# Performance work log

Hardware: AMD Instinct MI355X
Metric: run time of the kernel (lower is better)

The kernel has to match this reference:

```python
import jax, jax.numpy as jnp
import numpy as np

TEMP = 0.07
BATCH, DIM, NUM_ATTRS = 8192, 512, 4
NUM_PROTOS = 2 ** NUM_ATTRS  # all binary combos present => unique() size is static


def setup_inputs() -> dict:
    key = jax.random.key(0)
    z_flowed = jax.random.normal(key, (BATCH, DIM), dtype=jnp.float32)
    # binary attribute combos, all 16 present; first column = MSB (matches torch.unique row sort)
    combo = jnp.arange(BATCH, dtype=jnp.int32) % NUM_PROTOS
    shifts = jnp.arange(NUM_ATTRS - 1, -1, -1, dtype=jnp.int32)
    attributes = ((combo[:, None] >> shifts[None, :]) & 1).astype(jnp.float32)
    return {"z_flowed": z_flowed, "attributes": attributes}


def _l2norm(x, axis=-1, eps=1e-12):
    n = jnp.sqrt(jnp.sum(x * x, axis=axis, keepdims=True))
    return x / jnp.maximum(n, eps)  # F.normalize semantics


def reference(z_flowed, attributes):
    B, D = z_flowed.shape
    num_attrs = attributes.shape[1]
    P = 2 ** num_attrs
    z_norm = _l2norm(z_flowed, axis=1)

    # inverse indices of torch.unique(attributes, dim=0): binary row -> code (MSB = col 0)
    shifts = jnp.arange(num_attrs - 1, -1, -1)
    inverse = jnp.sum((attributes > 0.5).astype(jnp.int32) * (1 << shifts)[None, :], axis=1)

    # prototype = normalized segment-mean of z_norm per attribute combo (detached)
    sums = jax.ops.segment_sum(z_norm, inverse, num_segments=P)          # [P, D]
    counts = jax.ops.segment_sum(jnp.ones((B,), z_norm.dtype), inverse, num_segments=P)
    means = sums / jnp.maximum(counts, 1.0)[:, None]
    prototypes = jax.lax.stop_gradient(_l2norm(means, axis=1))
    prototypes = jnp.where(counts[:, None] > 0, prototypes, 0.0)

    # prototype contrastive term
    proto_sim = (z_norm @ prototypes.T) / TEMP                            # [B, P]
    exp_sim = jnp.exp(proto_sim)
    pos = exp_sim[jnp.arange(B), inverse]
    alls = jnp.maximum(jnp.sum(exp_sim, axis=1), 1e-8)
    loss = -jnp.mean(jnp.log(pos / alls + 1e-8))

    # pairwise term (positives only when BOTH attribute rows are all-ones)
    pairwise = (z_norm @ z_norm.T) / TEMP                                 # [B, B]
    attr_sim = attributes @ attributes.T
    pos_mask = (attr_sim == num_attrs).astype(z_norm.dtype)
    pos_mask = pos_mask * (1.0 - jnp.eye(B, dtype=z_norm.dtype))
    exp_pw = jnp.exp(pairwise)
    pos_sims = jnp.sum(exp_pw * pos_mask, axis=1)
    all_sims = jnp.sum(exp_pw, axis=1) - jnp.diagonal(exp_pw)
    valid = jnp.sum(pos_mask, axis=1) > 0
    per_row = -jnp.log(pos_sims / (all_sims + 1e-8) + 1e-8)
    n_valid = jnp.sum(valid.astype(z_norm.dtype))
    pairwise_loss = jnp.sum(jnp.where(valid, per_row, 0.0)) / jnp.maximum(n_valid, 1.0)
    loss = jnp.where(n_valid > 0, 0.7 * loss + 0.3 * pairwise_loss, loss)
    return loss
```

## Files before the change

### kernel.cpp

```cpp
#include <hip/hip_runtime.h>
#include <math.h>

#define NB 8192
#define ND 512
#define NPROTO 16
#define NBLK 256
#define TINV 14.285714285714286f
#define PW_BLOCKS 256
#define PL_BLOCKS 256

typedef short short8 __attribute__((ext_vector_type(8)));
typedef float float4v __attribute__((ext_vector_type(4)));

__device__ __forceinline__ unsigned short f2bf(float f) {
  unsigned u = __builtin_bit_cast(unsigned, f);
  unsigned r = (u + 0x7FFFu + ((u >> 16) & 1u)) >> 16;
  return (unsigned short)r;
}
__device__ __forceinline__ float bflo(unsigned u) {
  return __builtin_bit_cast(float, u << 16);
}
__device__ __forceinline__ float bfhi(unsigned u) {
  return __builtin_bit_cast(float, u & 0xFFFF0000u);
}

__global__ __launch_bounds__(512) void k_norm(
    const float* __restrict__ z, const float* __restrict__ attr,
    unsigned short* __restrict__ znb, float* __restrict__ partialSum,
    int* __restrict__ code, float* __restrict__ protoSumG)
{
  __shared__ float acc[NPROTO * ND];
  const int t = threadIdx.x, lane = t & 63, wid = t >> 6;
  for (int i = t; i < NPROTO * ND; i += 512) acc[i] = 0.f;
  if (blockIdx.x == 0)
    for (int i = t; i < NPROTO * ND; i += 512) protoSumG[i] = 0.f;
  __syncthreads();
  #pragma unroll
  for (int rr = 0; rr < 4; ++rr) {
    const int r = blockIdx.x * 32 + wid * 4 + rr;
    const float* zr = z + (size_t)r * ND;
    float v[8];
    #pragma unroll
    for (int jj = 0; jj < 8; ++jj) v[jj] = zr[lane + jj * 64];
    float s = 0.f;
    #pragma unroll
    for (int jj = 0; jj < 8; ++jj) s += v[jj] * v[jj];
    #pragma unroll
    for (int o = 32; o > 0; o >>= 1) s += __shfl_xor(s, o);
    const float inv = 1.f / fmaxf(sqrtf(s), 1e-12f);
    const float* a = attr + (size_t)r * 4;
    const int c = (a[0] > 0.5f ? 8 : 0) | (a[1] > 0.5f ? 4 : 0) |
                  (a[2] > 0.5f ? 2 : 0) | (a[3] > 0.5f ? 1 : 0);
    float* accRow = acc + c * ND;
    #pragma unroll
    for (int jj = 0; jj < 8; ++jj) {
      const float zv = v[jj] * inv;
      atomicAdd(&accRow[lane + jj * 64], zv);
      znb[(size_t)r * ND + lane + jj * 64] = f2bf(zv);
    }
    if (lane == 0) code[r] = c;
  }
  __syncthreads();
  for (int i = t; i < NPROTO * ND; i += 512) {
    const int p = i >> 9, d = i & 511;
    partialSum[(size_t)((p << 8) | blockIdx.x) * ND + d] = acc[i];
  }
}

__global__ __launch_bounds__(256) void k_reduce1(
    const float* __restrict__ partialSum, const int* __restrict__ code,
    float* __restrict__ protoSumG, int* __restrict__ validList,
    int* __restrict__ validCnt)
{
  const int t = threadIdx.x;
  if (blockIdx.x < 256) {
    const int p = blockIdx.x >> 4, c = blockIdx.x & 15;
    const float* base = partialSum + (size_t)(p * NBLK + c * 16) * ND;
    float s0 = 0.f, s1 = 0.f;
    #pragma unroll
    for (int k = 0; k < 16; ++k) {
      s0 += base[k * ND + t];
      s1 += base[k * ND + t + 256];
    }
    atomicAdd(&protoSumG[p * ND + t], s0);
    atomicAdd(&protoSumG[p * ND + t + 256], s1);
  } else {
    __shared__ int lcnt;
    if (t == 0) lcnt = 0;
    __syncthreads();
    for (int r = t; r < NB; r += 256) {
      if (code[r] == NPROTO - 1) {
        const int s = atomicAdd(&lcnt, 1);
        validList[s] = r;
      }
    }
    __syncthreads();
    if (t == 0) validCnt[0] = lcnt;
  }
}

#define PLD (ND + 4)
#define SMEM_BYTES 41472
__global__ __launch_bounds__(512) void k_main(
    const unsigned short* __restrict__ znb, const float* __restrict__ protoSumG,
    const int* __restrict__ code, const int* __restrict__ validList,
    const int* __restrict__ validCnt,
    float* __restrict__ partialAll, float* __restrict__ partialPos,
    float* __restrict__ plPart)
{
  __shared__ __align__(16) char smem[SMEM_BYTES];
  __shared__ float red3[8];
  __shared__ float gSh[16];
  const int t = threadIdx.x, lane = t & 63, wid = t >> 6;
  const int bi = blockIdx.x;
  if (bi < PW_BLOCKS) {
    unsigned short* aT = (unsigned short*)smem;
    unsigned short* bT = aT + 64 * 64;
    int* rowIdx = (int*)(bT + 256 * 64);
    unsigned char* aoSh = (unsigned char*)(rowIdx + 64);
    const int wv = wid >> 2, ww = wid & 3;
    const int m = validCnt[0];
    const int nIT = (m + 63) >> 6;
    const int items = nIT * 32;
    const int grp = lane >> 4, cl = lane & 15;
    for (int wi = bi; wi < items; wi += PW_BLOCKS) {
      const int i0 = (wi >> 5) * 64;
      const int jt = wi & 31;
      const int jb = jt * 256;
      __syncthreads();
      if (t < 64) rowIdx[t] = (i0 + t < m) ? validList[i0 + t] : -1;
      if (t < 256) aoSh[t] = (code[jb + t] == NPROTO - 1) ? 1 : 0;
      float4v acc[2][4];
      #pragma unroll
      for (int mi = 0; mi < 2; ++mi)
        #pragma unroll
        for (int nj = 0; nj < 4; ++nj) acc[mi][nj] = (float4v)(0.f);
      for (int kc = 0; kc < 8; ++kc) {
        const int k0 = kc * 64;
        __syncthreads();
        {
          const int ia = t >> 3, kq = t & 7;
          const int ri = rowIdx[ia];
          const int srow = (ri < 0) ? 0 : ri;
          const uint4 v = *(const uint4*)(znb + (size_t)srow * ND + k0 + kq * 8);
          *(uint4*)((char*)aT + ia * 128 + ((kq * 16) ^ ((ia & 7) << 4))) = v;
        }
        #pragma unroll
        for (int h = 0; h < 4; ++h) {
          const int f = t + h * 512;
          const int j = f >> 3, kq = f & 7;
          const uint4 v = *(const uint4*)(znb + (size_t)(jb + j) * ND + k0 + kq * 8);
          *(uint4*)((char*)bT + j * 128 + ((kq * 16) ^ ((j & 7) << 4))) = v;
        }
        __syncthreads();
        #pragma unroll
        for (int ks = 0; ks < 2; ++ks) {
          const int kb = ks * 64 + grp * 16;
          short8 af[2], bf[4];
          #pragma unroll
          for (int mi = 0; mi < 2; ++mi) {
            const int rw = wv * 32 + mi * 16 + cl;
            af[mi] = *(const short8*)((char*)aT + rw * 128 + (kb ^ ((rw & 7) << 4)));
          }
          #pragma unroll
          for (int nj = 0; nj < 4; ++nj) {
            const int rw = ww * 64 + nj * 16 + cl;
            bf[nj] = *(const short8*)((char*)bT + rw * 128 + (kb ^ ((rw & 7) << 4)));
          }
          #pragma unroll
          for (int mi = 0; mi < 2; ++mi)
            #pragma unroll
            for (int nj = 0; nj < 4; ++nj)
              acc[mi][nj] = __builtin_amdgcn_mfma_f32_16x16x32_bf16(af[mi], bf[nj], acc[mi][nj], 0, 0, 0);
        }
      }
      #pragma unroll
      for (int mi = 0; mi < 2; ++mi) {
        float sA[4] = {0.f, 0.f, 0.f, 0.f}, sP[4] = {0.f, 0.f, 0.f, 0.f};
        int ri[4];
        #pragma unroll
        for (int q = 0; q < 4; ++q) ri[q] = rowIdx[wv * 32 + mi * 16 + grp * 4 + q];
        #pragma unroll
        for (int nj = 0; nj < 4; ++nj) {
          const int jl = ww * 64 + nj * 16 + cl;
          const int jg = jb + jl;
          const float ao = aoSh[jl] ? 1.f : 0.f;
          #pragma unroll
          for (int q = 0; q < 4; ++q) {
            float e = __expf(acc[mi][nj][q] * TINV);
            e = (jg == ri[q]) ? 0.f : e;
            sA[q] += e;
            sP[q] += e * ao;
          }
        }
        #pragma unroll
        for (int q = 0; q < 4; ++q) {
          #pragma unroll
          for (int o = 1; o < 16; o <<= 1) {
            sA[q] += __shfl_xor(sA[q], o);
            sP[q] += __shfl_xor(sP[q], o);
          }
        }
        if (cl == 0) {
          const int slot0 = i0 + wv * 32 + mi * 16 + grp * 4;
          const int jt2 = jt * 4 + ww;
          if (slot0 + 3 < m) {
            *(float4*)&partialAll[(size_t)jt2 * NB + slot0] =
                make_float4(sA[0], sA[1], sA[2], sA[3]);
            *(float4*)&partialPos[(size_t)jt2 * NB + slot0] =
                make_float4(sP[0], sP[1], sP[2], sP[3]);
          } else {
            #pragma unroll
            for (int q = 0; q < 4; ++q) {
              if (slot0 + q < m) {
                partialAll[(size_t)jt2 * NB + slot0 + q] = sA[q];
                partialPos[(size_t)jt2 * NB + slot0 + q] = sP[q];
              }
            }
          }
        }
      }
    }
  } else {
    float* pl = (float*)smem;
    const int pb = bi - PW_BLOCKS;
    for (int i = t; i < NPROTO * ND; i += 512)
      pl[(i >> 9) * PLD + (i & 511)] = protoSumG[i];
    __syncthreads();
    {
      const int p = t >> 5, l32 = t & 31;
      float sq = 0.f;
      #pragma unroll
      for (int k = 0; k < 16; ++k) {
        const float v = pl[p * PLD + l32 + k * 32];
        sq += v * v;
      }
      #pragma unroll
      for (int o = 1; o < 32; o <<= 1) sq += __shfl_xor(sq, o);
      if (l32 == 0) gSh[p] = 1.f / fmaxf(sqrtf(sq), 1e-12f);
    }
    __syncthreads();
    for (int i = t; i < NPROTO * ND; i += 512)
      pl[(i >> 9) * PLD + (i & 511)] *= gSh[i >> 9];
    __syncthreads();
    const int p = lane & 15, grp = lane >> 4;
    float lacc = 0.f;
    #pragma unroll
    for (int rr = 0; rr < 4; ++rr) {
      const int r = pb * 32 + wid * 4 + rr;
      const uint4* zr = (const uint4*)(znb + (size_t)r * ND + grp * 128);
      const float* pbp = &pl[p * PLD + grp * 128];
      float s = 0.f;
      #pragma unroll
      for (int it = 0; it < 16; ++it) {
        const uint4 u = zr[it];
        const float4 p0 = *(const float4*)(pbp + it * 8);
        const float4 p1 = *(const float4*)(pbp + it * 8 + 4);
        s += bflo(u.x)*p0.x + bfhi(u.x)*p0.y + bflo(u.y)*p0.z + bfhi(u.y)*p0.w;
        s += bflo(u.z)*p1.x + bfhi(u.z)*p1.y + bflo(u.w)*p1.z + bfhi(u.w)*p1.w;
      }
      s += __shfl_xor(s, 16);
      s += __shfl_xor(s, 32);
      const float e = __expf(s * TINV);
      float alls = e;
      alls += __shfl_xor(alls, 1);
      alls += __shfl_xor(alls, 2);
      alls += __shfl_xor(alls, 4);
      alls += __shfl_xor(alls, 8);
      const int c = code[r];
      const float pos = __shfl(e, (lane & ~15) | c);
      if (lane == 0) lacc += -logf(pos / fmaxf(alls, 1e-8f) + 1e-8f);
    }
    if (lane == 0) red3[wid] = lacc;
    __syncthreads();
    if (t == 0)
      plPart[pb] = red3[0]+red3[1]+red3[2]+red3[3]+red3[4]+red3[5]+red3[6]+red3[7];
  }
}

__global__ __launch_bounds__(1024) void k_final(
    const float* __restrict__ partialAll, const float* __restrict__ partialPos,
    const float* __restrict__ plPart, const int* __restrict__ validCnt,
    float* __restrict__ out)
{
  __shared__ float shA[1024], shP[1024];
  __shared__ float red[16], red2[16];
  const int t = threadIdx.x, lane = t & 63, wid = t >> 6;
  const int m = validCnt[0];
  const int nvalid = (m >= 2) ? m : 0;
  const int slot = t & 511, half = t >> 9;
  float sa = 0.f, sp = 0.f;
  if (slot < nvalid) {
    const int k0 = half * 64;
    #pragma unroll 8
    for (int k = k0; k < k0 + 64; ++k) {
      sa += partialAll[(size_t)k * NB + slot];
      sp += partialPos[(size_t)k * NB + slot];
    }
  }
  shA[t] = sa; shP[t] = sp;
  __syncthreads();
  float s = 0.f;
  if (t < 512 && slot < nvalid) {
    const float A = shA[t] + shA[t + 512];
    const float P = shP[t] + shP[t + 512];
    s = -logf(P / (A + 1e-8f) + 1e-8f);
  }
  float pls = (t < PL_BLOCKS) ? plPart[t] : 0.f;
  #pragma unroll
  for (int o = 32; o > 0; o >>= 1) {
    s += __shfl_xor(s, o);
    pls += __shfl_xor(pls, o);
  }
  if (lane == 0) { red[wid] = s; red2[wid] = pls; }
  __syncthreads();
  if (t == 0) {
    float total = 0.f, plTot = 0.f;
    #pragma unroll
    for (int w = 0; w < 16; ++w) { total += red[w]; plTot += red2[w]; }
    const float proto = plTot / (float)NB;
    float loss = proto;
    if (nvalid > 0) loss = 0.7f * proto + 0.3f * (total / (float)nvalid);
    out[0] = loss;
  }
}

extern "C" void kernel_launch(void* const* d_in, const int* in_sizes, int n_in,
                              void* d_out, int out_size, void* d_ws, size_t ws_size,
                              hipStream_t stream) {
  const float* z = (const float*)d_in[0];
  const float* attr = (const float*)d_in[1];
  unsigned short* znb = (unsigned short*)d_ws;
  float* partialSum = (float*)(znb + (size_t)NB * ND);
  float* partialAll = partialSum;
  float* partialPos = partialSum + (size_t)128 * NB;
  char* w = (char*)(partialSum + (size_t)NBLK * NPROTO * ND);
  float* protoSumG = (float*)w;     w += NPROTO * ND * 4;
  int* validCnt = (int*)w;          w += 16;
  int* code = (int*)w;              w += NB * 4;
  int* validList = (int*)w;         w += NB * 4;
  float* plPart = (float*)w;        w += PL_BLOCKS * 4;
  k_norm<<<dim3(NBLK), dim3(512), 0, stream>>>(z, attr, znb, partialSum, code,
                                               protoSumG);
  k_reduce1<<<dim3(257), dim3(256), 0, stream>>>(partialSum, code, protoSumG,
                                                 validList, validCnt);
  k_main<<<dim3(PW_BLOCKS + PL_BLOCKS), dim3(512), 0, stream>>>(
      znb, protoSumG, code, validList, validCnt, partialAll, partialPos, plPart);
  k_final<<<dim3(1), dim3(1024), 0, stream>>>(partialAll, partialPos, plPart,
                                              validCnt, (float*)d_out);
}
```

Before: 72.05 us.

## Fuse four kernels into one persistent kernel with software grid barriers

Merges the normalize, reduce, main and final kernels into a single 256-block launch that is separated by atomic-counter grid barriers, and adds a memset of the barrier state. The goal is to remove the per-launch overhead and the gaps between kernels. The valid-list construction moves into the normalize phase using a global atomic, and the final reduction is spread across all blocks. In exchange, the barriers rely on all blocks being resident at once, and the pairwise and prototype phases now run one after the other in each block instead of on separate blocks.

```diff
diff --git a/kernel.cpp b/kernel.cpp
--- a/kernel.cpp
+++ b/kernel.cpp
@@ -4,10 +4,10 @@
 #define NB 8192
 #define ND 512
 #define NPROTO 16
-#define NBLK 256
+#define GRID 256
 #define TINV 14.285714285714286f
-#define PW_BLOCKS 256
-#define PL_BLOCKS 256
+#define PLD (ND + 4)
+#define SMEM_BYTES 41472
 
 typedef short short8 __attribute__((ext_vector_type(8)));
 typedef float float4v __attribute__((ext_vector_type(4)));
@@ -24,106 +24,111 @@
   return __builtin_bit_cast(float, u & 0xFFFF0000u);
 }
 
-__global__ __launch_bounds__(512) void k_norm(
+__device__ __forceinline__ void gridBar(unsigned* bs, int b) {
+  __syncthreads();
+  if (threadIdx.x == 0) {
+    __threadfence();
+    unsigned* cnt  = bs + b * 32;
+    unsigned* flag = bs + b * 32 + 16;
+    const unsigned o = atomicAdd(cnt, 1u);
+    if (o == (unsigned)(GRID - 1))
+      __hip_atomic_store(flag, 1u, __ATOMIC_RELEASE, __HIP_MEMORY_SCOPE_AGENT);
+    int spins = 0;
+    while (__hip_atomic_load(flag, __ATOMIC_RELAXED,
+                             __HIP_MEMORY_SCOPE_AGENT) == 0u) {
+      __builtin_amdgcn_s_sleep(2);
+      if (++spins > (1 << 22)) break;
+    }
+    __threadfence();
+  }
+  __syncthreads();
+}
+
+__global__ __launch_bounds__(512) void k_fused(
     const float* __restrict__ z, const float* __restrict__ attr,
-    unsigned short* __restrict__ znb, float* __restrict__ partialSum,
-    int* __restrict__ code, float* __restrict__ protoSumG)
-{
-  __shared__ float acc[NPROTO * ND];
-  const int t = threadIdx.x, lane = t & 63, wid = t >> 6;
-  for (int i = t; i < NPROTO * ND; i += 512) acc[i] = 0.f;
-  if (blockIdx.x == 0)
-    for (int i = t; i < NPROTO * ND; i += 512) protoSumG[i] = 0.f;
-  __syncthreads();
-  #pragma unroll
-  for (int rr = 0; rr < 4; ++rr) {
-    const int r = blockIdx.x * 32 + wid * 4 + rr;
-    const float* zr = z + (size_t)r * ND;
-    float v[8];
-    #pragma unroll
-    for (int jj = 0; jj < 8; ++jj) v[jj] = zr[lane + jj * 64];
-    float s = 0.f;
-    #pragma unroll
-    for (int jj = 0; jj < 8; ++jj) s += v[jj] * v[jj];
-    #pragma unroll
-    for (int o = 32; o > 0; o >>= 1) s += __shfl_xor(s, o);
-    const float inv = 1.f / fmaxf(sqrtf(s), 1e-12f);
-    const float* a = attr + (size_t)r * 4;
-    const int c = (a[0] > 0.5f ? 8 : 0) | (a[1] > 0.5f ? 4 : 0) |
-                  (a[2] > 0.5f ? 2 : 0) | (a[3] > 0.5f ? 1 : 0);
-    float* accRow = acc + c * ND;
-    #pragma unroll
-    for (int jj = 0; jj < 8; ++jj) {
-      const float zv = v[jj] * inv;
-      atomicAdd(&accRow[lane + jj * 64], zv);
-      znb[(size_t)r * ND + lane + jj * 64] = f2bf(zv);
-    }
-    if (lane == 0) code[r] = c;
-  }
-  __syncthreads();
-  for (int i = t; i < NPROTO * ND; i += 512) {
-    const int p = i >> 9, d = i & 511;
-    partialSum[(size_t)((p << 8) | blockIdx.x) * ND + d] = acc[i];
-  }
-}
-
-__global__ __launch_bounds__(256) void k_reduce1(
-    const float* __restrict__ partialSum, const int* __restrict__ code,
-    float* __restrict__ protoSumG, int* __restrict__ validList,
-    int* __restrict__ validCnt)
-{
-  const int t = threadIdx.x;
-  if (blockIdx.x < 256) {
-    const int p = blockIdx.x >> 4, c = blockIdx.x & 15;
-    const float* base = partialSum + (size_t)(p * NBLK + c * 16) * ND;
-    float s0 = 0.f, s1 = 0.f;
-    #pragma unroll
-    for (int k = 0; k < 16; ++k) {
-      s0 += base[k * ND + t];
-      s1 += base[k * ND + t + 256];
-    }
-    atomicAdd(&protoSumG[p * ND + t], s0);
-    atomicAdd(&protoSumG[p * ND + t + 256], s1);
-  } else {
-    __shared__ int lcnt;
-    if (t == 0) lcnt = 0;
-    __syncthreads();
-    for (int r = t; r < NB; r += 256) {
-      if (code[r] == NPROTO - 1) {
-        const int s = atomicAdd(&lcnt, 1);
-        validList[s] = r;
-      }
-    }
-    __syncthreads();
-    if (t == 0) validCnt[0] = lcnt;
-  }
-}
-
-#define PLD (ND + 4)
-#define SMEM_BYTES 41472
-__global__ __launch_bounds__(512) void k_main(
-    const unsigned short* __restrict__ znb, const float* __restrict__ protoSumG,
-    const int* __restrict__ code, const int* __restrict__ validList,
-    const int* __restrict__ validCnt,
-    float* __restrict__ partialAll, float* __restrict__ partialPos,
-    float* __restrict__ plPart)
+    unsigned short* __restrict__ znb,
+    float* __restrict__ partialSum,
+    float* __restrict__ protoSumG,
+    int* __restrict__ code, int* __restrict__ validList,
+    unsigned* __restrict__ barState,
+    float* __restrict__ partialAll,
+    float* __restrict__ partialPos,
+    float* __restrict__ plPart,
+    float* __restrict__ blockLoss,
+    float* __restrict__ out)
 {
   __shared__ __align__(16) char smem[SMEM_BYTES];
-  __shared__ float red3[8];
+  __shared__ float redS[8];
+  __shared__ float red2S[8];
   __shared__ float gSh[16];
   const int t = threadIdx.x, lane = t & 63, wid = t >> 6;
   const int bi = blockIdx.x;
-  if (bi < PW_BLOCKS) {
+  int* validCnt = (int*)(barState + 128);
+
+  {
+    float* acc = (float*)smem;
+    for (int i = t; i < NPROTO * ND; i += 512) acc[i] = 0.f;
+    if (bi == 0)
+      for (int i = t; i < NPROTO * ND; i += 512) protoSumG[i] = 0.f;
+    __syncthreads();
+    #pragma unroll
+    for (int rr = 0; rr < 4; ++rr) {
+      const int r = bi * 32 + wid * 4 + rr;
+      const float4* zr4 = (const float4*)(z + (size_t)r * ND);
+      const float4 va = zr4[lane];
+      const float4 vb = zr4[lane + 64];
+      float v[8] = {va.x, va.y, va.z, va.w, vb.x, vb.y, vb.z, vb.w};
+      float s = 0.f;
+      #pragma unroll
+      for (int k = 0; k < 8; ++k) s += v[k] * v[k];
+      #pragma unroll
+      for (int o = 32; o > 0; o >>= 1) s += __shfl_xor(s, o);
+      const float inv = 1.f / fmaxf(sqrtf(s), 1e-12f);
+      const float* a = attr + (size_t)r * 4;
+      const int c = (a[0] > 0.5f ? 8 : 0) | (a[1] > 0.5f ? 4 : 0) |
+                    (a[2] > 0.5f ? 2 : 0) | (a[3] > 0.5f ? 1 : 0);
+      float* accRow = acc + c * ND;
+      #pragma unroll
+      for (int k = 0; k < 8; ++k) {
+        const float zv = v[k] * inv;
+        atomicAdd(&accRow[k * 64 + lane], zv);
+        znb[(size_t)r * ND + k * 64 + lane] = f2bf(zv);
+      }
+      if (lane == 0) {
+        code[r] = c;
+        if (c == NPROTO - 1) { const int sl = atomicAdd(validCnt, 1); validList[sl] = r; }
+      }
+    }
+    __syncthreads();
+    for (int i = t; i < NPROTO * ND; i += 512) {
+      const int p = i >> 9, d = i & 511;
+      partialSum[(size_t)((p << 8) | bi) * ND + d] = acc[i];
+    }
+  }
+  gridBar(barState, 0);
+
+  {
+    const int p = bi >> 4, c = bi & 15;
+    const float* base = partialSum + (size_t)(p * GRID + c * 16) * ND;
+    float s = 0.f;
+    #pragma unroll
+    for (int k = 0; k < 16; ++k) s += base[k * ND + t];
+    atomicAdd(&protoSumG[p * ND + t], s);
+  }
+  gridBar(barState, 1);
+
+  const int m = validCnt[0];
+
+  {
     unsigned short* aT = (unsigned short*)smem;
     unsigned short* bT = aT + 64 * 64;
     int* rowIdx = (int*)(bT + 256 * 64);
     unsigned char* aoSh = (unsigned char*)(rowIdx + 64);
     const int wv = wid >> 2, ww = wid & 3;
-    const int m = validCnt[0];
     const int nIT = (m + 63) >> 6;
     const int items = nIT * 32;
     const int grp = lane >> 4, cl = lane & 15;
-    for (int wi = bi; wi < items; wi += PW_BLOCKS) {
+    for (int wi = bi; wi < items; wi += GRID) {
       const int i0 = (wi >> 5) * 64;
       const int jt = wi & 31;
       const int jb = jt * 256;
@@ -221,9 +226,11 @@
         }
       }
     }
-  } else {
+  }
+  __syncthreads();
+
+  {
     float* pl = (float*)smem;
-    const int pb = bi - PW_BLOCKS;
     for (int i = t; i < NPROTO * ND; i += 512)
       pl[(i >> 9) * PLD + (i & 511)] = protoSumG[i];
     __syncthreads();
@@ -247,7 +254,7 @@
     float lacc = 0.f;
     #pragma unroll
     for (int rr = 0; rr < 4; ++rr) {
-      const int r = pb * 32 + wid * 4 + rr;
+      const int r = bi * 32 + wid * 4 + rr;
       const uint4* zr = (const uint4*)(znb + (size_t)r * ND + grp * 128);
       const float* pbp = &pl[p * PLD + grp * 128];
       float s = 0.f;
@@ -271,57 +278,56 @@
       const float pos = __shfl(e, (lane & ~15) | c);
       if (lane == 0) lacc += -logf(pos / fmaxf(alls, 1e-8f) + 1e-8f);
     }
-    if (lane == 0) red3[wid] = lacc;
+    if (lane == 0) redS[wid] = lacc;
     __syncthreads();
     if (t == 0)
-      plPart[pb] = red3[0]+red3[1]+red3[2]+red3[3]+red3[4]+red3[5]+red3[6]+red3[7];
-  }
-}
-
-__global__ __launch_bounds__(1024) void k_final(
-    const float* __restrict__ partialAll, const float* __restrict__ partialPos,
-    const float* __restrict__ plPart, const int* __restrict__ validCnt,
-    float* __restrict__ out)
-{
-  __shared__ float shA[1024], shP[1024];
-  __shared__ float red[16], red2[16];
-  const int t = threadIdx.x, lane = t & 63, wid = t >> 6;
-  const int m = validCnt[0];
-  const int nvalid = (m >= 2) ? m : 0;
-  const int slot = t & 511, half = t >> 9;
-  float sa = 0.f, sp = 0.f;
-  if (slot < nvalid) {
-    const int k0 = half * 64;
-    #pragma unroll 8
-    for (int k = k0; k < k0 + 64; ++k) {
-      sa += partialAll[(size_t)k * NB + slot];
-      sp += partialPos[(size_t)k * NB + slot];
-    }
-  }
-  shA[t] = sa; shP[t] = sp;
-  __syncthreads();
-  float s = 0.f;
-  if (t < 512 && slot < nvalid) {
-    const float A = shA[t] + shA[t + 512];
-    const float P = shP[t] + shP[t + 512];
-    s = -logf(P / (A + 1e-8f) + 1e-8f);
-  }
-  float pls = (t < PL_BLOCKS) ? plPart[t] : 0.f;
-  #pragma unroll
-  for (int o = 32; o > 0; o >>= 1) {
-    s += __shfl_xor(s, o);
-    pls += __shfl_xor(pls, o);
-  }
-  if (lane == 0) { red[wid] = s; red2[wid] = pls; }
-  __syncthreads();
-  if (t == 0) {
-    float total = 0.f, plTot = 0.f;
+      plPart[bi] = redS[0]+redS[1]+redS[2]+redS[3]+redS[4]+redS[5]+redS[6]+redS[7];
+  }
+  gridBar(barState, 2);
+
+  {
+    const int nvalid = (m >= 2) ? m : 0;
+    float bl = 0.f;
+    for (int s = bi * 8 + wid; s < nvalid; s += GRID * 8) {
+      float a = partialAll[(size_t)lane * NB + s] +
+                partialAll[(size_t)(lane + 64) * NB + s];
+      float p = partialPos[(size_t)lane * NB + s] +
+                partialPos[(size_t)(lane + 64) * NB + s];
+      #pragma unroll
+      for (int o = 32; o > 0; o >>= 1) {
+        a += __shfl_xor(a, o);
+        p += __shfl_xor(p, o);
+      }
+      if (lane == 0) bl += -logf(p / (a + 1e-8f) + 1e-8f);
+    }
+    __syncthreads();
+    if (lane == 0) redS[wid] = bl;
+    __syncthreads();
+    if (t == 0)
+      blockLoss[bi] = redS[0]+redS[1]+redS[2]+redS[3]+redS[4]+redS[5]+redS[6]+redS[7];
+  }
+  gridBar(barState, 3);
+
+  if (bi == 0) {
+    const int nvalid = (m >= 2) ? m : 0;
+    float s = (t < GRID) ? blockLoss[t] : 0.f;
+    float pls = (t < GRID) ? plPart[t] : 0.f;
     #pragma unroll
-    for (int w = 0; w < 16; ++w) { total += red[w]; plTot += red2[w]; }
-    const float proto = plTot / (float)NB;
-    float loss = proto;
-    if (nvalid > 0) loss = 0.7f * proto + 0.3f * (total / (float)nvalid);
-    out[0] = loss;
+    for (int o = 32; o > 0; o >>= 1) {
+      s += __shfl_xor(s, o);
+      pls += __shfl_xor(pls, o);
+    }
+    if (lane == 0) { redS[wid] = s; red2S[wid] = pls; }
+    __syncthreads();
+    if (t == 0) {
+      float total = 0.f, plTot = 0.f;
+      #pragma unroll
+      for (int w = 0; w < 8; ++w) { total += redS[w]; plTot += red2S[w]; }
+      const float proto = plTot / (float)NB;
+      float loss = proto;
+      if (nvalid > 0) loss = 0.7f * proto + 0.3f * (total / (float)nvalid);
+      out[0] = loss;
+    }
   }
 }
 
@@ -330,22 +336,19 @@
                               hipStream_t stream) {
   const float* z = (const float*)d_in[0];
   const float* attr = (const float*)d_in[1];
-  unsigned short* znb = (unsigned short*)d_ws;
-  float* partialSum = (float*)(znb + (size_t)NB * ND);
+  char* w = (char*)d_ws;
+  unsigned short* znb = (unsigned short*)w;  w += (size_t)NB * ND * 2;
+  float* partialSum = (float*)w;             w += (size_t)NPROTO * GRID * ND * 4;
   float* partialAll = partialSum;
   float* partialPos = partialSum + (size_t)128 * NB;
-  char* w = (char*)(partialSum + (size_t)NBLK * NPROTO * ND);
-  float* protoSumG = (float*)w;     w += NPROTO * ND * 4;
-  int* validCnt = (int*)w;          w += 16;
-  int* code = (int*)w;              w += NB * 4;
-  int* validList = (int*)w;         w += NB * 4;
-  float* plPart = (float*)w;        w += PL_BLOCKS * 4;
-  k_norm<<<dim3(NBLK), dim3(512), 0, stream>>>(z, attr, znb, partialSum, code,
-                                               protoSumG);
-  k_reduce1<<<dim3(257), dim3(256), 0, stream>>>(partialSum, code, protoSumG,
-                                                 validList, validCnt);
-  k_main<<<dim3(PW_BLOCKS + PL_BLOCKS), dim3(512), 0, stream>>>(
-      znb, protoSumG, code, validList, validCnt, partialAll, partialPos, plPart);
-  k_final<<<dim3(1), dim3(1024), 0, stream>>>(partialAll, partialPos, plPart,
-                                              validCnt, (float*)d_out);
-}
+  float* protoSumG = (float*)w;              w += NPROTO * ND * 4;
+  int* code = (int*)w;                       w += NB * 4;
+  int* validList = (int*)w;                  w += NB * 4;
+  float* plPart = (float*)w;                 w += GRID * 4;
+  float* blockLoss = (float*)w;              w += GRID * 4;
+  unsigned* barState = (unsigned*)w;         w += 1024;
+  hipMemsetAsync(barState, 0, 1024, stream);
+  k_fused<<<dim3(GRID), dim3(512), 0, stream>>>(
+      z, attr, znb, partialSum, protoSumG, code, validList, barState,
+      partialAll, partialPos, plPart, blockLoss, (float*)d_out);
+}
```

Result: slower. 135.3 us (+87.7%).
